# Performance work log

Hardware: AMD Instinct MI355X
Metric: run time of the kernel (lower is better)

Reference implementation:

```python
import jax, jax.numpy as jnp
import numpy as np

B = 1                 # images
GRID = 30             # patch grid per side (HEIGHT_FACTOR*2)
NIMG = GRID * GRID    # 900 tokens per image
EMBED = 1152
HEADS = 16
DH = EMBED // HEADS   # 72
DHH = DH // 2         # 36
LAYERS = 6
FF = 4608             # mlp intermediate (4*EMBED)
MERGE = 2
MHID = EMBED * MERGE * MERGE   # 4608 merger hidden
OUT = 2048
DS_IDX = (2, 5)
PS = 16               # spatial patch size
TP = 2                # temporal patch size
THETA = 10000.0


def _rope_cos_sin():
    # 2D rotary positions in merge-block order: (Hf, Wf, mh, mw)
    HF = GRID // MERGE
    I, J, MH, MW = np.meshgrid(np.arange(HF), np.arange(HF), np.arange(MERGE), np.arange(MERGE), indexing='ij')
    hpos = (I * MERGE + MH).reshape(-1).astype(np.float32)
    wpos = (J * MERGE + MW).reshape(-1).astype(np.float32)
    inv = 1.0 / (THETA ** (np.arange(0, DHH, 2, dtype=np.float32) / DHH))      # [DH//4]
    rot = np.concatenate([hpos[:, None] * inv, wpos[:, None] * inv], axis=-1)  # [NIMG, DHH]
    cos = np.concatenate([np.cos(rot), np.cos(rot)], axis=-1)[None, None]      # [1,1,NIMG,DH]
    sin = np.concatenate([np.sin(rot), np.sin(rot)], axis=-1)[None, None]
    return jnp.asarray(cos, jnp.float32), jnp.asarray(sin, jnp.float32)


def _ln(x, w, b, eps=1e-6):
    mu = x.mean(-1, keepdims=True)
    xc = x - mu
    v = (xc * xc).mean(-1, keepdims=True)
    return xc * jax.lax.rsqrt(v + eps) * w + b


def _rot_half(t):
    t1, t2 = jnp.split(t, 2, axis=-1)
    return jnp.concatenate([-t2, t1], axis=-1)


def setup_inputs():
    key = jax.random.key(0)
    ks = jax.random.split(key, 12)
    s = 0.02
    n = lambda k, sh: jax.random.normal(k, sh, jnp.float32) * s
    z = lambda sh: jnp.zeros(sh, jnp.float32)
    o = lambda sh: jnp.ones(sh, jnp.float32)
    cos, sin = _rope_cos_sin()
    return {
        'pixel_values': jax.random.uniform(ks[0], (B, 1, 3, GRID * PS, GRID * PS), jnp.float32) * 255.0,
        'patch_w': n(ks[1], (EMBED, 3 * TP * PS * PS)), 'patch_b': z((EMBED,)),
        'pos_emb': n(ks[2], (1, NIMG, EMBED)),
        'cos': cos, 'sin': sin,
        'ln1_w': o((LAYERS, EMBED)), 'ln1_b': z((LAYERS, EMBED)),
        'qkv_w': n(ks[3], (LAYERS, 3 * EMBED, EMBED)), 'qkv_b': z((LAYERS, 3 * EMBED)),
        'proj_w': n(ks[4], (LAYERS, EMBED, EMBED)), 'proj_b': z((LAYERS, EMBED)),
        'ln2_w': o((LAYERS, EMBED)), 'ln2_b': z((LAYERS, EMBED)),
        'fc1_w': n(ks[5], (LAYERS, FF, EMBED)), 'fc1_b': z((LAYERS, FF)),
        'fc2_w': n(ks[6], (LAYERS, EMBED, FF)), 'fc2_b': z((LAYERS, EMBED)),
        'ds_norm_w': o((2, MHID)), 'ds_norm_b': z((2, MHID)),
        'ds_fc1_w': n(ks[7], (2, MHID, MHID)), 'ds_fc1_b': z((2, MHID)),
        'ds_fc2_w': n(ks[8], (2, OUT, MHID)), 'ds_fc2_b': z((2, OUT)),
        'm_norm_w': o((EMBED,)), 'm_norm_b': z((EMBED,)),
        'm_fc1_w': n(ks[9], (MHID, MHID)), 'm_fc1_b': z((MHID,)),
        'm_fc2_w': n(ks[10], (OUT, MHID)), 'm_fc2_b': z((OUT,)),
    }


def _forward(pixel_values, patch_w, patch_b, pos_emb, cos, sin, ln1_w, ln1_b, qkv_w, qkv_b, proj_w, proj_b, ln2_w, ln2_b, fc1_w, fc1_b, fc2_w, fc2_b, ds_norm_w, ds_norm_b, ds_fc1_w, ds_fc1_b, ds_fc2_w, ds_fc2_b, m_norm_w, m_norm_b, m_fc1_w, m_fc1_b, m_fc2_w, m_fc2_b):
    HF = GRID // MERGE
    x = (pixel_values - 127.5) * (1.0 / 127.5)                 # [B,1,3,H,W]
    x = jnp.concatenate([x, x], axis=1)                        # temporal duplication -> [B,2,3,H,W]
    x = x.reshape(B, 1, TP, 3, HF, MERGE, PS, HF, MERGE, PS)
    x = jnp.transpose(x, (0, 1, 4, 7, 5, 8, 3, 2, 6, 9))       # [B,1,HF,WF,mh,mw,3,TP,ps,ps]
    x = x.reshape(-1, 3 * TP * PS * PS)                        # [B*NIMG, 1536] (conv3d == matmul)
    h = (x @ patch_w.T + patch_b).reshape(1, -1, EMBED)        # [1, N, E]
    N = B * NIMG
    h = h + jnp.tile(pos_emb, (1, B, 1))
    cosf = jnp.tile(cos, (1, 1, B, 1))                         # [1,1,N,DH]
    sinf = jnp.tile(sin, (1, 1, B, 1))
    ds = []
    for l in range(LAYERS):
        hn = _ln(h, ln1_w[l], ln1_b[l])
        qkv = (hn @ qkv_w[l].T + qkv_b[l]).reshape(N, 3, HEADS, DH)
        qkv = jnp.transpose(qkv, (1, 2, 0, 3))                 # [3, H, N, dh]
        q, k, v = qkv[0][None], qkv[1][None], qkv[2][None]     # [1, H, N, dh]
        q = q * cosf + _rot_half(q) * sinf                     # inline RoPE (q,k pre-scaled by dh**-0.25 in weights)
        k = k * cosf + _rot_half(k) * sinf
        qb = jnp.transpose(q[0].reshape(HEADS, B, NIMG, DH), (1, 0, 2, 3))  # per-image attention blocks
        kb = jnp.transpose(k[0].reshape(HEADS, B, NIMG, DH), (1, 0, 2, 3))
        vb = jnp.transpose(v[0].reshape(HEADS, B, NIMG, DH), (1, 0, 2, 3))
        attn = jax.nn.softmax(jnp.einsum('bhqd,bhkd->bhqk', qb, kb), axis=-1)
        o = jnp.einsum('bhqk,bhkd->bhqd', attn, vb)            # [B, H, NIMG, dh]
        o = jnp.transpose(o, (0, 2, 1, 3)).reshape(1, N, EMBED)
        h = h + (o @ proj_w[l].T + proj_b[l])
        m = jax.nn.gelu(_ln(h, ln2_w[l], ln2_b[l]) @ fc1_w[l].T + fc1_b[l], approximate=True)
        h = h + (m @ fc2_w[l].T + fc2_b[l])
        if l in DS_IDX:
            d = DS_IDX.index(l)
            xm = _ln(h.reshape(1, -1, MHID), ds_norm_w[d], ds_norm_b[d])
            xm = jax.nn.gelu(xm @ ds_fc1_w[d].T + ds_fc1_b[d], approximate=True) @ ds_fc2_w[d].T + ds_fc2_b[d]
            ds.append(xm)                                      # [1, N/4, OUT]
    hm = _ln(h, m_norm_w, m_norm_b).reshape(1, -1, MHID)
    out = jax.nn.gelu(hm @ m_fc1_w.T + m_fc1_b, approximate=True) @ m_fc2_w.T + m_fc2_b
    return ds, out


def reference(pixel_values, patch_w, patch_b, pos_emb, cos, sin, ln1_w, ln1_b, qkv_w, qkv_b, proj_w, proj_b, ln2_w, ln2_b, fc1_w, fc1_b, fc2_w, fc2_b, ds_norm_w, ds_norm_b, ds_fc1_w, ds_fc1_b, ds_fc2_w, ds_fc2_b, m_norm_w, m_norm_b, m_fc1_w, m_fc1_b, m_fc2_w, m_fc2_b):
    ds, out = _forward(pixel_values, patch_w, patch_b, pos_emb, cos, sin, ln1_w, ln1_b, qkv_w, qkv_b, proj_w, proj_b, ln2_w, ln2_b, fc1_w, fc1_b, fc2_w, fc2_b, ds_norm_w, ds_norm_b, ds_fc1_w, ds_fc1_b, ds_fc2_w, ds_fc2_b, m_norm_w, m_norm_b, m_fc1_w, m_fc1_b, m_fc2_w, m_fc2_b)
    return (*ds, out)
```

## Files before the change

kernel.cpp:

```cpp
#include <hip/hip_runtime.h>
#include <hip/hip_bf16.h>
#include <cstdint>

#define NT   900
#define EMB  1152
#define NH   16
#define DHD  72
#define DHH  36
#define DHP  96
#define KVP  928
#define NL   6
#define FFD  4608
#define MHD  4608
#define OUTD 2048
#define NM   225

typedef __attribute__((ext_vector_type(8))) short short8;
typedef __attribute__((ext_vector_type(4))) float f32x4;

__device__ __forceinline__ ushort f2bf(float f) {
    uint32_t u = __float_as_uint(f);
    uint32_t r = u + 0x7FFF + ((u >> 16) & 1);
    return (ushort)(r >> 16);
}
__device__ __forceinline__ float gelu_f(float x) {
    return 0.5f * x * (1.0f + tanhf(0.7978845608f * (x + 0.044715f * x * x * x)));
}

__global__ __launch_bounds__(256) void k_cvt(const float* __restrict__ src,
                                             ushort* __restrict__ dst, int n4) {
    int idx = blockIdx.x * 256 + threadIdx.x;
    if (idx >= n4) return;
    const float4 v = *(const float4*)(src + (size_t)idx * 4);
    ushort o[4] = { f2bf(v.x), f2bf(v.y), f2bf(v.z), f2bf(v.w) };
    *(uint2*)(dst + (size_t)idx * 4) = *(const uint2*)o;
}

__global__ __launch_bounds__(256) void k_patch(const float* __restrict__ pix,
                                               ushort* __restrict__ xp) {
    int idx = blockIdx.x * 256 + threadIdx.x;
    if (idx >= NT * 1536) return;
    int t = idx / 1536, f = idx - t * 1536;
    int mw = t & 1, mh = (t >> 1) & 1;
    int tq = t >> 2;
    int jj = tq % 15, ii = tq / 15;
    int pw = f & 15, ph = (f >> 4) & 15, c = f >> 9;
    int Hi = (ii * 2 + mh) * 16 + ph;
    int Wi = (jj * 2 + mw) * 16 + pw;
    float p = pix[((size_t)c * 480 + Hi) * 480 + Wi];
    xp[idx] = f2bf((p - 127.5f) * (1.0f / 127.5f));
}

__global__ __launch_bounds__(256) void k_ln(const float* __restrict__ x,
                                            const float* __restrict__ w,
                                            const float* __restrict__ b,
                                            ushort* __restrict__ y, int C) {
    int row = blockIdx.x;
    int tid = threadIdx.x;
    const float* xr = x + (size_t)row * C;
    float s = 0.f, ss = 0.f;
    for (int c = tid; c < C; c += 256) { float v = xr[c]; s += v; ss += v * v; }
    for (int off = 32; off; off >>= 1) {
        s  += __shfl_down(s,  off, 64);
        ss += __shfl_down(ss, off, 64);
    }
    __shared__ float rs[4], rss[4];
    int wid = tid >> 6, lane = tid & 63;
    if (lane == 0) { rs[wid] = s; rss[wid] = ss; }
    __syncthreads();
    float S  = rs[0] + rs[1] + rs[2] + rs[3];
    float SS = rss[0] + rss[1] + rss[2] + rss[3];
    float mu  = S / C;
    float var = SS / C - mu * mu;
    float inv = rsqrtf(var + 1e-6f);
    ushort* yr = y + (size_t)row * C;
    for (int c = tid; c < C; c += 256) yr[c] = f2bf((xr[c] - mu) * inv * w[c] + b[c]);
}

template <int ACT, int OBF16, int SPLIT>
__global__ __launch_bounds__(256) void k_bgs(const ushort* __restrict__ A,
                                             const ushort* __restrict__ W,
                                             const float* __restrict__ bias,
                                             const float* __restrict__ res,
                                             void* __restrict__ Cp,
                                             float* __restrict__ part,
                                             int M, int N, int K, int S) {
    __shared__ __align__(16) ushort As[64 * 72];
    __shared__ __align__(16) ushort Bs[64 * 72];
    int tid = threadIdx.x;
    int row0 = blockIdx.x * 64, col0 = blockIdx.y * 64;
    int z = blockIdx.z;
    int Kc = K / S;
    int kbeg = z * Kc;
    int steps = Kc >> 6;

    int srow = tid >> 2;
    int scol = (tid & 3) << 4;
    int ar = row0 + srow; if (ar > M - 1) ar = M - 1;
    int wr = col0 + srow;
    const ushort* aptr = A + (size_t)ar * K + kbeg + scol;
    const ushort* wptr = W + (size_t)wr * K + kbeg + scol;
    ushort* asd = &As[srow * 72 + scol];
    ushort* bsd = &Bs[srow * 72 + scol];

    uint4 ra0, ra1, rb0, rb1;
    auto loadchunk = [&](int s) {
        const ushort* p = aptr + (s << 6);
        ra0 = *(const uint4*)p; ra1 = *(const uint4*)(p + 8);
        const ushort* q = wptr + (s << 6);
        rb0 = *(const uint4*)q; rb1 = *(const uint4*)(q + 8);
    };

    int lane = tid & 63, wid = tid >> 6;
    int wrr = (wid >> 1) * 32, wcc = (wid & 1) * 32;
    int fr = lane & 15, kg8 = (lane >> 4) << 3;

    f32x4 acc[2][2] = {};
    loadchunk(0);
    for (int s = 0; s < steps; ++s) {
        __syncthreads();
        *(uint4*)asd = ra0; *(uint4*)(asd + 8) = ra1;
        *(uint4*)bsd = rb0; *(uint4*)(bsd + 8) = rb1;
        if (s + 1 < steps) loadchunk(s + 1);
        __syncthreads();
#pragma unroll
        for (int j = 0; j < 2; ++j) {
            int ko = j * 32 + kg8;
            short8 a0 = *(const short8*)&As[(wrr + fr) * 72 + ko];
            short8 a1 = *(const short8*)&As[(wrr + 16 + fr) * 72 + ko];
            short8 b0 = *(const short8*)&Bs[(wcc + fr) * 72 + ko];
            short8 b1 = *(const short8*)&Bs[(wcc + 16 + fr) * 72 + ko];
            acc[0][0] = __builtin_amdgcn_mfma_f32_16x16x32_bf16(a0, b0, acc[0][0], 0, 0, 0);
            acc[0][1] = __builtin_amdgcn_mfma_f32_16x16x32_bf16(a0, b1, acc[0][1], 0, 0, 0);
            acc[1][0] = __builtin_amdgcn_mfma_f32_16x16x32_bf16(a1, b0, acc[1][0], 0, 0, 0);
            acc[1][1] = __builtin_amdgcn_mfma_f32_16x16x32_bf16(a1, b1, acc[1][1], 0, 0, 0);
        }
    }

#pragma unroll
    for (int fi = 0; fi < 2; fi++)
#pragma unroll
        for (int fj = 0; fj < 2; fj++)
#pragma unroll
            for (int r = 0; r < 4; r++) {
                int row = row0 + wrr + fi * 16 + (lane >> 4) * 4 + r;
                int col = col0 + wcc + fj * 16 + fr;
                if (row < M) {
                    if (SPLIT) {
                        part[((size_t)z * M + row) * N + col] = acc[fi][fj][r];
                    } else {
                        float v = acc[fi][fj][r] + bias[col];
                        if (res) v += res[(size_t)row * N + col];
                        if (ACT == 1) v = gelu_f(v);
                        if (OBF16) ((ushort*)Cp)[(size_t)row * N + col] = f2bf(v);
                        else       ((float*)Cp)[(size_t)row * N + col] = v;
                    }
                }
            }
}

template <int ACT, int OBF16>
__global__ __launch_bounds__(256) void k_fix(const float* __restrict__ part,
                                             const float* __restrict__ bias,
                                             const float* __restrict__ res,
                                             void* __restrict__ Cp,
                                             int M, int N, int S) {
    size_t idx = (size_t)blockIdx.x * 256 + threadIdx.x;
    size_t total = (size_t)M * N / 4;
    if (idx >= total) return;
    size_t e = idx * 4;
    int row = (int)(e / N), col = (int)(e - (size_t)row * N);
    float4 v = *(const float4*)(part + e);
    for (int s = 1; s < S; ++s) {
        const float4 p = *(const float4*)(part + (size_t)s * M * N + e);
        v.x += p.x; v.y += p.y; v.z += p.z; v.w += p.w;
    }
    const float4 bi = *(const float4*)(bias + col);
    v.x += bi.x; v.y += bi.y; v.z += bi.z; v.w += bi.w;
    if (res) {
        const float4 rr = *(const float4*)(res + e);
        v.x += rr.x; v.y += rr.y; v.z += rr.z; v.w += rr.w;
    }
    if (ACT == 1) { v.x = gelu_f(v.x); v.y = gelu_f(v.y); v.z = gelu_f(v.z); v.w = gelu_f(v.w); }
    if (OBF16) {
        ushort o[4] = { f2bf(v.x), f2bf(v.y), f2bf(v.z), f2bf(v.w) };
        *(uint2*)((ushort*)Cp + e) = *(const uint2*)o;
    } else {
        *(float4*)((float*)Cp + e) = v;
    }
}

template <int OBF16>
__global__ __launch_bounds__(256) void k_mm(const ushort* __restrict__ A,
                                            const ushort* __restrict__ Wb,
                                            void* __restrict__ Cp,
                                            int M, int N, int K, int ldc, int Nw,
                                            long as_, long ws_, long cs_) {
    __shared__ __align__(16) ushort As[64 * 40];
    __shared__ __align__(16) ushort Bs[64 * 40];
    int z = blockIdx.z;
    A  += (size_t)z * as_;
    Wb += (size_t)z * ws_;
    float*  Cf = (float*)Cp + (size_t)z * cs_;
    ushort* Cb = (ushort*)Cp + (size_t)z * cs_;

    int tid = threadIdx.x;
    int row0 = blockIdx.y * 64, col0 = blockIdx.x * 64;

    int sm = tid >> 2, sp = tid & 3;
    int ar = row0 + sm; if (ar > M - 1) ar = M - 1;
    int wr = col0 + sm; if (wr > N - 1) wr = N - 1;
    const ushort* aptr = A + (size_t)ar * K;

    int lane = tid & 63, wid = tid >> 6;
    int wrr = (wid >> 1) * 32, wcc = (wid & 1) * 32;
    int fr = lane & 15, kg = lane >> 4;

    f32x4 acc[2][2] = {};

    for (int k0 = 0; k0 < K; k0 += 32) {
        *(uint4*)&As[sm * 40 + sp * 8] = *(const uint4*)(aptr + k0 + sp * 8);
        *(uint4*)&Bs[sm * 40 + sp * 8] = *(const uint4*)(Wb + (size_t)wr * K + k0 + sp * 8);
        __syncthreads();
        short8 a0 = *(const short8*)&As[(wrr + fr) * 40 + kg * 8];
        short8 a1 = *(const short8*)&As[(wrr + 16 + fr) * 40 + kg * 8];
        short8 b0 = *(const short8*)&Bs[(wcc + fr) * 40 + kg * 8];
        short8 b1 = *(const short8*)&Bs[(wcc + 16 + fr) * 40 + kg * 8];
        acc[0][0] = __builtin_amdgcn_mfma_f32_16x16x32_bf16(a0, b0, acc[0][0], 0, 0, 0);
        acc[0][1] = __builtin_amdgcn_mfma_f32_16x16x32_bf16(a0, b1, acc[0][1], 0, 0, 0);
        acc[1][0] = __builtin_amdgcn_mfma_f32_16x16x32_bf16(a1, b0, acc[1][0], 0, 0, 0);
        acc[1][1] = __builtin_amdgcn_mfma_f32_16x16x32_bf16(a1, b1, acc[1][1], 0, 0, 0);
        __syncthreads();
    }

#pragma unroll
    for (int fi = 0; fi < 2; fi++)
#pragma unroll
        for (int fj = 0; fj < 2; fj++)
#pragma unroll
            for (int r = 0; r < 4; r++) {
                int row = row0 + wrr + fi * 16 + (lane >> 4) * 4 + r;
                int col = col0 + wcc + fj * 16 + (lane & 15);
                if (row < M && col < Nw) {
                    float v = acc[fi][fj][r];
                    if (OBF16) Cb[(size_t)row * ldc + col] = f2bf(v);
                    else       Cf[(size_t)row * ldc + col] = v;
                }
            }
}

__global__ __launch_bounds__(256) void k_rope(const float* __restrict__ qkv,
                                              const float* __restrict__ cs,
                                              const float* __restrict__ sn,
                                              ushort* __restrict__ q,
                                              ushort* __restrict__ k,
                                              ushort* __restrict__ vt) {
    int idx = blockIdx.x * 256 + threadIdx.x;
    if (idx >= NT * NH * DHP) return;
    int t = idx / (NH * DHP);
    int rem = idx - t * (NH * DHP);
    int h = rem / DHP, d = rem - h * DHP;
    size_t oi = ((size_t)h * NT + t) * DHP + d;
    if (d < DHD) {
        const float* base = qkv + (size_t)t * 3 * EMB;
        float c = cs[t * DHD + d], s = sn[t * DHD + d];
        int   d2 = (d < DHH) ? d + DHH : d - DHH;
        float sg = (d < DHH) ? -1.f : 1.f;
        int e = h * DHD + d;
        float qv = base[e] * c + sg * base[h * DHD + d2] * s;
        float kv = base[EMB + e] * c + sg * base[EMB + h * DHD + d2] * s;
        q[oi] = f2bf(qv);
        k[oi] = f2bf(kv);
        vt[((size_t)h * DHP + d) * KVP + t] = f2bf(base[2 * EMB + e]);
    } else {
        q[oi] = 0;
        k[oi] = 0;
    }
}

__global__ __launch_bounds__(256) void k_vpad(ushort* __restrict__ vt) {
    int idx = blockIdx.x * 256 + threadIdx.x;
    int tot = NH * DHP * (KVP - NT);
    if (idx >= tot) return;
    int pw = KVP - NT;
    int hd = idx / pw, j = idx - hd * pw;
    vt[(size_t)hd * KVP + NT + j] = 0;
}

__global__ __launch_bounds__(256) void k_sm(const float* __restrict__ S,
                                            ushort* __restrict__ P) {
    int row = blockIdx.x * 4 + (threadIdx.x >> 6);
    int lane = threadIdx.x & 63;
    const float* sp = S + (size_t)row * KVP;
    ushort* pp = P + (size_t)row * KVP;
    float v[15];
#pragma unroll
    for (int i = 0; i < 15; i++) {
        int kt = lane + i * 64;
        v[i] = (kt < NT) ? sp[kt] : -1e30f;
    }
    float mx = -1e30f;
#pragma unroll
    for (int i = 0; i < 15; i++) mx = fmaxf(mx, v[i]);
    for (int off = 32; off; off >>= 1) mx = fmaxf(mx, __shfl_xor(mx, off, 64));
    float sum = 0.f;
#pragma unroll
    for (int i = 0; i < 15; i++) {
        int kt = lane + i * 64;
        v[i] = (kt < NT) ? __expf(v[i] - mx) : 0.f;
        sum += v[i];
    }
    for (int off = 32; off; off >>= 1) sum += __shfl_xor(sum, off, 64);
    float inv = 1.f / sum;
#pragma unroll
    for (int i = 0; i < 15; i++) {
        int kt = lane + i * 64;
        if (kt < KVP) pp[kt] = f2bf(v[i] * inv);
    }
}

extern "C" void kernel_launch(void* const* d_in, const int* in_sizes, int n_in,
                              void* d_out, int out_size, void* d_ws, size_t ws_size,
                              hipStream_t stream) {
    const float* pix     = (const float*)d_in[0];
    const float* patch_w = (const float*)d_in[1];
    const float* patch_b = (const float*)d_in[2];
    const float* pos_emb = (const float*)d_in[3];
    const float* cosb    = (const float*)d_in[4];
    const float* sinb    = (const float*)d_in[5];
    const float* ln1_w   = (const float*)d_in[6];
    const float* ln1_b   = (const float*)d_in[7];
    const float* qkv_w   = (const float*)d_in[8];
    const float* qkv_b   = (const float*)d_in[9];
    const float* proj_w  = (const float*)d_in[10];
    const float* proj_b  = (const float*)d_in[11];
    const float* ln2_w   = (const float*)d_in[12];
    const float* ln2_b   = (const float*)d_in[13];
    const float* fc1_w   = (const float*)d_in[14];
    const float* fc1_b   = (const float*)d_in[15];
    const float* fc2_w   = (const float*)d_in[16];
    const float* fc2_b   = (const float*)d_in[17];
    const float* dsn_w   = (const float*)d_in[18];
    const float* dsn_b   = (const float*)d_in[19];
    const float* ds1_w   = (const float*)d_in[20];
    const float* ds1_b   = (const float*)d_in[21];
    const float* ds2_w   = (const float*)d_in[22];
    const float* ds2_b   = (const float*)d_in[23];
    const float* mn_w    = (const float*)d_in[24];
    const float* mn_b    = (const float*)d_in[25];
    const float* mf1_w   = (const float*)d_in[26];
    const float* mf1_b   = (const float*)d_in[27];
    const float* mf2_w   = (const float*)d_in[28];
    const float* mf2_b   = (const float*)d_in[29];
    float* out = (float*)d_out;

    float* wsf = (float*)d_ws;
    size_t off = 0;
    auto af = [&](size_t n) { float* p = wsf + off; off += (n + 3) & ~(size_t)3; return p; };
    float* h    = af((size_t)NT * EMB);
    float* qkv  = af((size_t)NT * 3 * EMB);
    float* part = af((size_t)4 * NT * EMB);
    float* S    = af((size_t)NH * NT * KVP);
    ushort* wsh = (ushort*)(wsf + off);
    size_t hoff = 0;
    auto ah = [&](size_t n) { ushort* p = wsh + hoff; hoff += (n + 7) & ~(size_t)7; return p; };
    ushort* hn  = ah((size_t)NT * EMB);
    ushort* qb  = ah((size_t)NH * NT * DHP);
    ushort* kb  = ah((size_t)NH * NT * DHP);
    ushort* vt  = ah((size_t)NH * DHP * KVP);
    ushort* P   = ah((size_t)NH * NT * KVP);
    ushort* ob  = ah((size_t)NT * EMB);
    ushort* t1  = ah((size_t)NT * FFD);
    ushort* xp  = t1;
    ushort* w_patch = ah((size_t)EMB * 1536);
    ushort* w_qkv   = ah((size_t)NL * 3 * EMB * EMB);
    ushort* w_proj  = ah((size_t)NL * EMB * EMB);
    ushort* w_fc1   = ah((size_t)NL * FFD * EMB);
    ushort* w_fc2   = ah((size_t)NL * EMB * FFD);
    ushort* w_ds1   = ah((size_t)2 * MHD * MHD);
    ushort* w_ds2   = ah((size_t)2 * OUTD * MHD);
    ushort* w_mf1   = ah((size_t)MHD * MHD);
    ushort* w_mf2   = ah((size_t)OUTD * MHD);

    const long QS = (long)NT * DHP;
    const long VS = (long)DHP * KVP;
    const long SS = (long)NT * KVP;

    const int MB  = (NT + 63) / 64;
    const int MBm = (NM + 63) / 64;
    auto fixg = [](int M, int N) { return dim3(((size_t)M * N / 4 + 255) / 256); };
    auto cvt = [&](const float* s, ushort* d, size_t n) {
        k_cvt<<<dim3((unsigned)((n / 4 + 255) / 256)), 256, 0, stream>>>(s, d, (int)(n / 4));
    };

    cvt(patch_w, w_patch, (size_t)EMB * 1536);
    cvt(qkv_w,   w_qkv,   (size_t)NL * 3 * EMB * EMB);
    cvt(proj_w,  w_proj,  (size_t)NL * EMB * EMB);
    cvt(fc1_w,   w_fc1,   (size_t)NL * FFD * EMB);
    cvt(fc2_w,   w_fc2,   (size_t)NL * EMB * FFD);
    cvt(ds1_w,   w_ds1,   (size_t)2 * MHD * MHD);
    cvt(ds2_w,   w_ds2,   (size_t)2 * OUTD * MHD);
    cvt(mf1_w,   w_mf1,   (size_t)MHD * MHD);
    cvt(mf2_w,   w_mf2,   (size_t)OUTD * MHD);

    k_patch<<<dim3((NT * 1536 + 255) / 256), 256, 0, stream>>>(pix, xp);
    k_vpad<<<dim3((NH * DHP * (KVP - NT) + 255) / 256), 256, 0, stream>>>(vt);
    k_bgs<0, 0, 1><<<dim3(MB, EMB / 64, 2), 256, 0, stream>>>(
        xp, w_patch, nullptr, nullptr, nullptr, part, NT, EMB, 1536, 2);
    k_fix<0, 0><<<fixg(NT, EMB), 256, 0, stream>>>(part, patch_b, pos_emb, h, NT, EMB, 2);

    for (int l = 0; l < NL; ++l) {
        k_ln<<<NT, 256, 0, stream>>>(h, ln1_w + l * EMB, ln1_b + l * EMB, hn, EMB);
        k_bgs<0, 0, 0><<<dim3(MB, 3 * EMB / 64, 1), 256, 0, stream>>>(
            hn, w_qkv + (size_t)l * 3 * EMB * EMB, qkv_b + l * 3 * EMB, nullptr, qkv,
            nullptr, NT, 3 * EMB, EMB, 1);
        k_rope<<<dim3((NT * NH * DHP + 255) / 256), 256, 0, stream>>>(
            qkv, cosb, sinb, qb, kb, vt);
        k_mm<0><<<dim3(MB, MB, NH), 256, 0, stream>>>(
            qb, kb, S, NT, NT, DHP, KVP, NT, QS, QS, SS);
        k_sm<<<dim3(NH * NT / 4), 256, 0, stream>>>(S, P);
        k_mm<1><<<dim3(2, MB, NH), 256, 0, stream>>>(
            P, vt, ob, NT, DHD, KVP, EMB, DHD, SS, VS, DHD);
        k_bgs<0, 0, 1><<<dim3(MB, EMB / 64, 3), 256, 0, stream>>>(
            ob, w_proj + (size_t)l * EMB * EMB, nullptr, nullptr, nullptr, part,
            NT, EMB, EMB, 3);
        k_fix<0, 0><<<fixg(NT, EMB), 256, 0, stream>>>(part, proj_b + l * EMB, h, h,
                                                       NT, EMB, 3);
        k_ln<<<NT, 256, 0, stream>>>(h, ln2_w + l * EMB, ln2_b + l * EMB, hn, EMB);
        k_bgs<1, 1, 0><<<dim3(MB, FFD / 64, 1), 256, 0, stream>>>(
            hn, w_fc1 + (size_t)l * FFD * EMB, fc1_b + l * FFD, nullptr, t1,
            nullptr, NT, FFD, EMB, 1);
        k_bgs<0, 0, 1><<<dim3(MB, EMB / 64, 4), 256, 0, stream>>>(
            t1, w_fc2 + (size_t)l * EMB * FFD, nullptr, nullptr, nullptr, part,
            NT, EMB, FFD, 4);
        k_fix<0, 0><<<fixg(NT, EMB), 256, 0, stream>>>(part, fc2_b + l * EMB, h, h,
                                                       NT, EMB, 4);
        if (l == 2 || l == 5) {
            int d = (l == 2) ? 0 : 1;
            k_ln<<<NM, 256, 0, stream>>>(h, dsn_w + d * MHD, dsn_b + d * MHD, hn, MHD);
            k_bgs<0, 0, 1><<<dim3(MBm, MHD / 64, 4), 256, 0, stream>>>(
                hn, w_ds1 + (size_t)d * MHD * MHD, nullptr, nullptr, nullptr, part,
                NM, MHD, MHD, 4);
            k_fix<1, 1><<<fixg(NM, MHD), 256, 0, stream>>>(part, ds1_b + d * MHD,
                                                           nullptr, t1, NM, MHD, 4);
            k_bgs<0, 0, 1><<<dim3(MBm, OUTD / 64, 4), 256, 0, stream>>>(
                t1, w_ds2 + (size_t)d * OUTD * MHD, nullptr, nullptr, nullptr, part,
                NM, OUTD, MHD, 4);
            k_fix<0, 0><<<fixg(NM, OUTD), 256, 0, stream>>>(
                part, ds2_b + d * OUTD, nullptr, out + (size_t)d * NM * OUTD,
                NM, OUTD, 4);
        }
    }
    k_ln<<<NT, 256, 0, stream>>>(h, mn_w, mn_b, hn, EMB);
    k_bgs<0, 0, 1><<<dim3(MBm, MHD / 64, 4), 256, 0, stream>>>(
        hn, w_mf1, nullptr, nullptr, nullptr, part, NM, MHD, MHD, 4);
    k_fix<1, 1><<<fixg(NM, MHD), 256, 0, stream>>>(part, mf1_b, nullptr, t1, NM, MHD, 4);
    k_bgs<0, 0, 1><<<dim3(MBm, OUTD / 64, 4), 256, 0, stream>>>(
        t1, w_mf2, nullptr, nullptr, nullptr, part, NM, OUTD, MHD, 4);
    k_fix<0, 0><<<fixg(NM, OUTD), 256, 0, stream>>>(
        part, mf2_b, nullptr, out + (size_t)2 * NM * OUTD, NM, OUTD, 4);
}
```

Baseline: 1.499 ms.

## Load GEMM tiles directly into LDS with XOR-swizzled layout

Replaces the register-staged global-to-LDS copy in the bf16 GEMM with 16-byte global_load_lds instructions that write straight into shared memory. The padded 72-stride tiles become unpadded 64-stride tiles with an XOR swizzle on the 8-element column groups, so LDS bank conflicts stay low without padding. This removes the VGPR round trip and the LDS store instructions. It also drops the register prefetch of the next k-chunk, so global loads no longer overlap the MFMA work of the current chunk.

```diff
diff --git a/kernel.cpp b/kernel.cpp
--- a/kernel.cpp
+++ b/kernel.cpp
@@ -25,6 +25,12 @@
 }
 __device__ __forceinline__ float gelu_f(float x) {
     return 0.5f * x * (1.0f + tanhf(0.7978845608f * (x + 0.044715f * x * x * x)));
+}
+
+__device__ __forceinline__ void g2lds16(const ushort* g, ushort* l) {
+    __builtin_amdgcn_global_load_lds(
+        (const __attribute__((address_space(1))) unsigned int*)g,
+        (__attribute__((address_space(3))) unsigned int*)l, 16, 0, 0);
 }
 
 __global__ __launch_bounds__(256) void k_cvt(const float* __restrict__ src,
@@ -85,8 +91,8 @@
                                              void* __restrict__ Cp,
                                              float* __restrict__ part,
                                              int M, int N, int K, int S) {
-    __shared__ __align__(16) ushort As[64 * 72];
-    __shared__ __align__(16) ushort Bs[64 * 72];
+    __shared__ __align__(16) ushort As[64 * 64];
+    __shared__ __align__(16) ushort Bs[64 * 64];
     int tid = threadIdx.x;
     int row0 = blockIdx.x * 64, col0 = blockIdx.y * 64;
     int z = blockIdx.z;
@@ -94,42 +100,44 @@
     int kbeg = z * Kc;
     int steps = Kc >> 6;
 
-    int srow = tid >> 2;
-    int scol = (tid & 3) << 4;
-    int ar = row0 + srow; if (ar > M - 1) ar = M - 1;
-    int wr = col0 + srow;
-    const ushort* aptr = A + (size_t)ar * K + kbeg + scol;
-    const ushort* wptr = W + (size_t)wr * K + kbeg + scol;
-    ushort* asd = &As[srow * 72 + scol];
-    ushort* bsd = &Bs[srow * 72 + scol];
-
-    uint4 ra0, ra1, rb0, rb1;
-    auto loadchunk = [&](int s) {
-        const ushort* p = aptr + (s << 6);
-        ra0 = *(const uint4*)p; ra1 = *(const uint4*)(p + 8);
-        const ushort* q = wptr + (s << 6);
-        rb0 = *(const uint4*)q; rb1 = *(const uint4*)(q + 8);
-    };
-
-    int lane = tid & 63, wid = tid >> 6;
-    int wrr = (wid >> 1) * 32, wcc = (wid & 1) * 32;
+    int w = tid >> 6, lane = tid & 63;
+    int lrow = lane >> 3;
+    int cg   = ((lane & 7) ^ lrow) << 3;
+
+    int ar0 = row0 + w * 16 + lrow; if (ar0 > M - 1) ar0 = M - 1;
+    int ar1 = row0 + w * 16 + 8 + lrow; if (ar1 > M - 1) ar1 = M - 1;
+    int wr0 = col0 + w * 16 + lrow;
+    int wr1 = wr0 + 8;
+    const ushort* ap0 = A + (size_t)ar0 * K + kbeg + cg;
+    const ushort* ap1 = A + (size_t)ar1 * K + kbeg + cg;
+    const ushort* wp0 = W + (size_t)wr0 * K + kbeg + cg;
+    const ushort* wp1 = W + (size_t)wr1 * K + kbeg + cg;
+    ushort* asd0 = &As[(w * 16) * 64];
+    ushort* asd1 = &As[(w * 16 + 8) * 64];
+    ushort* bsd0 = &Bs[(w * 16) * 64];
+    ushort* bsd1 = &Bs[(w * 16 + 8) * 64];
+
     int fr = lane & 15, kg8 = (lane >> 4) << 3;
+    int wrr = (w >> 1) * 32, wcc = (w & 1) * 32;
+    int sw = (fr & 7) << 3;
 
     f32x4 acc[2][2] = {};
-    loadchunk(0);
     for (int s = 0; s < steps; ++s) {
+        int kk = s << 6;
         __syncthreads();
-        *(uint4*)asd = ra0; *(uint4*)(asd + 8) = ra1;
-        *(uint4*)bsd = rb0; *(uint4*)(bsd + 8) = rb1;
-        if (s + 1 < steps) loadchunk(s + 1);
+        g2lds16(ap0 + kk, asd0);
+        g2lds16(ap1 + kk, asd1);
+        g2lds16(wp0 + kk, bsd0);
+        g2lds16(wp1 + kk, bsd1);
         __syncthreads();
 #pragma unroll
         for (int j = 0; j < 2; ++j) {
             int ko = j * 32 + kg8;
-            short8 a0 = *(const short8*)&As[(wrr + fr) * 72 + ko];
-            short8 a1 = *(const short8*)&As[(wrr + 16 + fr) * 72 + ko];
-            short8 b0 = *(const short8*)&Bs[(wcc + fr) * 72 + ko];
-            short8 b1 = *(const short8*)&Bs[(wcc + 16 + fr) * 72 + ko];
+            int kx = ko ^ sw;
+            short8 a0 = *(const short8*)&As[(wrr + fr) * 64 + kx];
+            short8 a1 = *(const short8*)&As[(wrr + 16 + fr) * 64 + kx];
+            short8 b0 = *(const short8*)&Bs[(wcc + fr) * 64 + kx];
+            short8 b1 = *(const short8*)&Bs[(wcc + 16 + fr) * 64 + kx];
             acc[0][0] = __builtin_amdgcn_mfma_f32_16x16x32_bf16(a0, b0, acc[0][0], 0, 0, 0);
             acc[0][1] = __builtin_amdgcn_mfma_f32_16x16x32_bf16(a0, b1, acc[0][1], 0, 0, 0);
             acc[1][0] = __builtin_amdgcn_mfma_f32_16x16x32_bf16(a1, b0, acc[1][0], 0, 0, 0);
```

Result: no change. 1.484 ms (-0.9%).
